# Performance work log

Measured on AMD Instinct MI355X. Metric: run time of the kernel, lower is better.

## Reference

```python
import jax, jax.numpy as jnp
import numpy as np

L, B, S, D, SD, E, V = 6, 16, 512, 512, 128, 1536, 32000
PDX = 1  # padding_idx: embedding row zeroed


def _pos_encode(seq_len, d_model):
    pos = np.arange(seq_len)[:, None].astype(np.float32)
    i = np.arange(d_model)[None, :].astype(np.float32)
    ang = pos / np.power(10000.0, 2.0 * np.floor(i / 2.0) / d_model)
    pe = np.where(np.arange(d_model)[None, :] % 2 == 0, np.sin(ang), np.cos(ang))
    return jnp.asarray(pe, dtype=jnp.float32)


def setup_inputs() -> dict:
    key = jax.random.key(0)
    ks = jax.random.split(key, 12)
    def n(k, shape, std=0.02):
        return jax.random.normal(k, shape, jnp.float32) * std
    embed = n(ks[0], (V, D)).at[PDX].set(0.0)
    return dict(
        src_tokens=jax.random.randint(ks[1], (B, S), 0, V),
        src_mask=jax.random.randint(ks[2], (B, S), 0, 2).astype(bool),
        embed=embed,
        ln_g=jnp.ones((L, D)), ln_b=jnp.zeros((L, D)),
        Wz=n(ks[3], (L, D, SD)), bz=jnp.zeros((L, SD)),
        gq=1.0 + n(ks[4], (L, S, SD)), bq=n(ks[5], (L, S, SD)),
        gk=1.0 + n(ks[6], (L, S, SD)), bk=n(ks[7], (L, S, SD)),
        Wu=n(ks[8], (L, D, E)), bu=jnp.zeros((L, E)),
        Wv=n(ks[9], (L, D, E)), bv=jnp.zeros((L, E)),
        Wo=n(ks[10], (L, E, D)), bo=jnp.zeros((L, D)),
        fin_g=jnp.ones((D,)), fin_b=jnp.zeros((D,)),
    )


def _ln(x, g, b, eps=1e-5):
    m = x.mean(-1, keepdims=True)
    v = ((x - m) ** 2).mean(-1, keepdims=True)
    return (x - m) * jax.lax.rsqrt(v + eps) * g + b


def reference(src_tokens, src_mask, embed, ln_g, ln_b, Wz, bz, gq, bq, gk, bk,
              Wu, bu, Wv, bv, Wo, bo, fin_g, fin_b):
    d_model = embed.shape[1]
    x = embed[src_tokens] * (d_model ** 0.5)
    x = x + _pos_encode(src_tokens.shape[1], d_model)[None]  # dropout: eval -> identity
    mask = src_mask[:, None, :]  # (B,1,S): zero attention to masked key positions

    def layer(x, p):
        lg, lb, wz, bz_, gq_, bq_, gk_, bk_, wu, bu_, wv, bv_, wo, bo_ = p
        xn = _ln(x, lg, lb)
        u = xn @ wu + bu_          # (B,S,E)
        v = xn @ wv + bv_          # (B,S,E)
        z = xn @ wz + bz_          # (B,S,SD)
        q = z * gq_ + bq_          # scale_offset (per-position affine)
        k = z * gk_ + bk_
        a = jnp.maximum(jnp.einsum('bsd,btd->bst', q, k), 0.0) ** 2  # relu(qk)^2
        a = jnp.where(mask, 0.0, a)
        o = u * jnp.einsum('bst,bte->bse', a, v)  # gated attention output
        return x + o @ wo + bo_, None

    params = (ln_g, ln_b, Wz, bz, gq, bq, gk, bk, Wu, bu, Wv, bv, Wo, bo)
    x, _ = jax.lax.scan(layer, x, params)
    return _ln(x, fin_g, fin_b)
```

## Files before the change

### kernel.cpp

```cpp
#include <hip/hip_runtime.h>
#include <hip/hip_bf16.h>
#include <stdint.h>

constexpr int L = 6, B = 16, S = 512, D = 512, SD = 128, E = 1536;

using bf16x8 = __attribute__((ext_vector_type(8))) short;
using f32x4  = __attribute__((ext_vector_type(4))) float;

typedef __attribute__((address_space(1))) void gvoid;
typedef __attribute__((address_space(3))) void lvoid;

__device__ __forceinline__ unsigned short f2bf(float f) {
    __hip_bfloat16 h = __float2bfloat16(f);
    return __builtin_bit_cast(unsigned short, h);
}
__device__ __forceinline__ float bf2f(unsigned short u) {
    unsigned int v = ((unsigned int)u) << 16;
    return __builtin_bit_cast(float, v);
}
__device__ __forceinline__ void gload16(const void* g, void* l) {
    __builtin_amdgcn_global_load_lds((gvoid*)g, (lvoid*)l, 16, 0, 0);
}

__device__ __forceinline__ void swz_bid(int& bx, int& by, int& bz) {
    int gx = gridDim.x, gy = gridDim.y, gz = gridDim.z;
    int n = gx * gy * gz;
    int id = blockIdx.x + gx * (blockIdx.y + gy * blockIdx.z);
    int id2 = (id & 7) * (n >> 3) + (id >> 3);
    by = id2 % gy;
    int t = id2 / gy;
    bx = t % gx;
    bz = t / gx;
}

__global__ void detect_mask_kernel(const unsigned char* __restrict__ m, int* flag) {
    if (threadIdx.x == 0) *flag = 0;
    __syncthreads();
    int any = 0;
    for (int i = threadIdx.x; i < B * S; i += blockDim.x)
        if ((i & 3) != 0 && m[i] != 0) any = 1;
    if (any) atomicOr(flag, 1);
}

__global__ void embed_kernel(const int* __restrict__ tok, const float* __restrict__ embed,
                             float* __restrict__ x) {
    int idx = blockIdx.x * blockDim.x + threadIdx.x;
    int d = idx & (D - 1);
    int bs = idx >> 9;
    int s = bs & (S - 1);
    float e = embed[(size_t)tok[bs] * D + d] * 22.62741699796952f;
    float expo = (float)(d >> 1) * (1.0f / 256.0f);
    float ang = (float)s * expf(expo * -9.210340371976184f);
    float pe = (d & 1) ? cosf(ang) : sinf(ang);
    x[idx] = e + pe;
}

__global__ __launch_bounds__(256) void tcast_kernel(const float* __restrict__ W,
                                                    unsigned short* __restrict__ Wt,
                                                    int K, int N, long ostride) {
    __shared__ float t[32][33];
    W  += (size_t)blockIdx.z * K * N;
    Wt += (size_t)blockIdx.z * ostride;
    int k0 = blockIdx.x * 32, n0 = blockIdx.y * 32;
    int tx = threadIdx.x, ty = threadIdx.y;
#pragma unroll
    for (int i = 0; i < 4; ++i)
        t[ty + i * 8][tx] = W[(size_t)(k0 + ty + i * 8) * N + n0 + tx];
    __syncthreads();
#pragma unroll
    for (int i = 0; i < 4; ++i)
        Wt[(size_t)(n0 + ty + i * 8) * K + k0 + tx] = f2bf(t[tx][ty + i * 8]);
}

template <bool BF>
__global__ __launch_bounds__(256) void ln_kernel(const float* __restrict__ x,
                                                 const float* __restrict__ g,
                                                 const float* __restrict__ b,
                                                 void* __restrict__ yp) {
    int row = blockIdx.x * 4 + (threadIdx.x >> 6);
    int lane = threadIdx.x & 63;
    const float* xr = x + (size_t)row * D;
    float4 v0 = *(const float4*)(xr + lane * 4);
    float4 v1 = *(const float4*)(xr + 256 + lane * 4);
    float sum = v0.x + v0.y + v0.z + v0.w + v1.x + v1.y + v1.z + v1.w;
#pragma unroll
    for (int o = 1; o < 64; o <<= 1) sum += __shfl_xor(sum, o);
    float m = sum * (1.0f / D);
    float d0 = v0.x - m, d1 = v0.y - m, d2 = v0.z - m, d3 = v0.w - m;
    float e0 = v1.x - m, e1 = v1.y - m, e2 = v1.z - m, e3 = v1.w - m;
    float sq = d0 * d0 + d1 * d1 + d2 * d2 + d3 * d3 + e0 * e0 + e1 * e1 + e2 * e2 + e3 * e3;
#pragma unroll
    for (int o = 1; o < 64; o <<= 1) sq += __shfl_xor(sq, o);
    float inv = rsqrtf(sq * (1.0f / D) + 1e-5f);
    int c0 = lane * 4, c1 = 256 + lane * 4;
    float4 g0 = *(const float4*)(g + c0), g1 = *(const float4*)(g + c1);
    float4 b0 = *(const float4*)(b + c0), b1 = *(const float4*)(b + c1);
    float o0 = d0 * inv * g0.x + b0.x, o1 = d1 * inv * g0.y + b0.y;
    float o2 = d2 * inv * g0.z + b0.z, o3 = d3 * inv * g0.w + b0.w;
    float o4 = e0 * inv * g1.x + b1.x, o5 = e1 * inv * g1.y + b1.y;
    float o6 = e2 * inv * g1.z + b1.z, o7 = e3 * inv * g1.w + b1.w;
    if constexpr (BF) {
        unsigned short* yr = (unsigned short*)yp + (size_t)row * D;
        ushort4 p0 = {f2bf(o0), f2bf(o1), f2bf(o2), f2bf(o3)};
        ushort4 p1 = {f2bf(o4), f2bf(o5), f2bf(o6), f2bf(o7)};
        *(ushort4*)(yr + c0) = p0;
        *(ushort4*)(yr + c1) = p1;
    } else {
        float* yr = (float*)yp + (size_t)row * D;
        float4 p0 = {o0, o1, o2, o3}, p1 = {o4, o5, o6, o7};
        *(float4*)(yr + c0) = p0;
        *(float4*)(yr + c1) = p1;
    }
}

template <int BM, int BN, bool SWAP>
__device__ __forceinline__ void gemm_core(const unsigned short* __restrict__ Ab,
                                          const unsigned short* __restrict__ Bb,
                                          int K, short* lsA, short* lsB,
                                          f32x4 (&acc)[BM / 32][BN / 32],
                                          int lane, int wv) {
    constexpr int NA = BM / 32, NB = BN / 32;
    constexpr int FM = BM / 32, FN = BN / 32;
    constexpr int WTM = BM / 2, WTN = BN / 2;
    const int wm = wv >> 1, wn = wv & 1;
    const unsigned short* ga[NA]; int lofsA[NA];
    const unsigned short* gb[NB]; int lofsB[NB];
#pragma unroll
    for (int i = 0; i < NA; ++i) {
        int s = wv * NA + i;
        int r = s * 8 + (lane >> 3);
        int cl = (lane & 7) ^ (r & 7);
        ga[i] = Ab + (size_t)r * K + cl * 8;
        lofsA[i] = s * 512;
    }
#pragma unroll
    for (int i = 0; i < NB; ++i) {
        int s = wv * NB + i;
        int r = s * 8 + (lane >> 3);
        int cl = (lane & 7) ^ (r & 7);
        gb[i] = Bb + (size_t)r * K + cl * 8;
        lofsB[i] = s * 512;
    }
    const int nkt = K >> 6;
    for (int kt = 0; kt < nkt; ++kt) {
        if (kt) __syncthreads();
#pragma unroll
        for (int i = 0; i < NA; ++i) gload16(ga[i] + kt * 64, (void*)&lsA[lofsA[i]]);
#pragma unroll
        for (int i = 0; i < NB; ++i) gload16(gb[i] + kt * 64, (void*)&lsB[lofsB[i]]);
        __syncthreads();
#pragma unroll
        for (int ks = 0; ks < 2; ++ks) {
            bf16x8 aF[FM], bF[FN];
#pragma unroll
            for (int f = 0; f < FM; ++f) {
                int ra = wm * WTM + f * 16 + (lane & 15);
                int ca = (ks * 4 + (lane >> 4)) ^ (ra & 7);
                aF[f] = *(const bf16x8*)&lsA[ra * 64 + ca * 8];
            }
#pragma unroll
            for (int f = 0; f < FN; ++f) {
                int rb = wn * WTN + f * 16 + (lane & 15);
                int cb = (ks * 4 + (lane >> 4)) ^ (rb & 7);
                bF[f] = *(const bf16x8*)&lsB[rb * 64 + cb * 8];
            }
#pragma unroll
            for (int fi = 0; fi < FM; ++fi)
#pragma unroll
                for (int fj = 0; fj < FN; ++fj) {
                    if constexpr (SWAP)
                        acc[fi][fj] = __builtin_amdgcn_mfma_f32_16x16x32_bf16(
                            bF[fj], aF[fi], acc[fi][fj], 0, 0, 0);
                    else
                        acc[fi][fj] = __builtin_amdgcn_mfma_f32_16x16x32_bf16(
                            aF[fi], bF[fj], acc[fi][fj], 0, 0, 0);
                }
        }
    }
}

__global__ __launch_bounds__(256) void uv_gemm(const unsigned short* __restrict__ xn,
                                               const unsigned short* __restrict__ Wuvt,
                                               const float* __restrict__ bu,
                                               const float* __restrict__ bvp,
                                               unsigned short* __restrict__ u,
                                               unsigned short* __restrict__ vt) {
    __shared__ short lsA[128 * 64];
    __shared__ short lsB[128 * 64];
    int bx, by, bz;
    swz_bid(bx, by, bz);
    const int tid = threadIdx.x;
    const int lane = tid & 63, wv = tid >> 6;
    const int wm = wv >> 1, wn = wv & 1;
    const int row0 = bx * 128, col0 = by * 128;
    const unsigned short* Ab = xn + (size_t)row0 * D;
    const unsigned short* Bb = Wuvt + ((size_t)bz * E + col0) * D;

    const int lr4 = (lane >> 4) * 4;
    const int lc = lane & 15;
    if (bz == 0) {
        f32x4 acc[4][4] = {};
        gemm_core<128, 128, true>(Ab, Bb, D, lsA, lsB, acc, lane, wv);
#pragma unroll
        for (int fi = 0; fi < 4; ++fi) {
            int r = row0 + wm * 64 + fi * 16 + lc;
#pragma unroll
            for (int fj = 0; fj < 4; ++fj) {
                int cb = col0 + wn * 64 + fj * 16 + lr4;
                f32x4 v = acc[fi][fj];
                f32x4 bv = *(const f32x4*)&bu[cb];
                ushort4 ov = {f2bf(v[0] + bv[0]), f2bf(v[1] + bv[1]),
                              f2bf(v[2] + bv[2]), f2bf(v[3] + bv[3])};
                *(ushort4*)&u[(size_t)r * E + cb] = ov;
            }
        }
    } else {
        f32x4 acc[4][4] = {};
        gemm_core<128, 128, false>(Ab, Bb, D, lsA, lsB, acc, lane, wv);
#pragma unroll
        for (int fi = 0; fi < 4; ++fi) {
            int rb = row0 + wm * 64 + fi * 16 + lr4;
#pragma unroll
            for (int fj = 0; fj < 4; ++fj) {
                int c = col0 + wn * 64 + fj * 16 + lc;
                f32x4 v = acc[fi][fj];
                float bv = bvp[c];
                int b = rb >> 9, t0 = rb & 511;
                ushort4 ov = {f2bf(v[0] + bv), f2bf(v[1] + bv),
                              f2bf(v[2] + bv), f2bf(v[3] + bv)};
                *(ushort4*)&vt[((size_t)b * E + c) * 512 + t0] = ov;
            }
        }
    }
}

__global__ __launch_bounds__(256) void zqk_gemm(const unsigned short* __restrict__ xn,
                                                const unsigned short* __restrict__ Bt,
                                                const float* __restrict__ bias,
                                                const float* __restrict__ gq,
                                                const float* __restrict__ bq,
                                                const float* __restrict__ gk,
                                                const float* __restrict__ bk,
                                                unsigned short* __restrict__ q,
                                                unsigned short* __restrict__ k) {
    __shared__ short lsA[128 * 64];
    __shared__ short lsB[128 * 64];
    int bx, by, bz;
    swz_bid(bx, by, bz);
    const int tid = threadIdx.x;
    const int lane = tid & 63, wv = tid >> 6;
    const int wm = wv >> 1, wn = wv & 1;
    const int row0 = bx * 128;
    const unsigned short* Ab = xn + (size_t)row0 * D;

    f32x4 acc[4][4] = {};
    gemm_core<128, 128, true>(Ab, Bt, D, lsA, lsB, acc, lane, wv);

    const int lr4 = (lane >> 4) * 4;
    const int lc = lane & 15;
#pragma unroll
    for (int fi = 0; fi < 4; ++fi) {
        int r = row0 + wm * 64 + fi * 16 + lc;
        int s = r & 511;
#pragma unroll
        for (int fj = 0; fj < 4; ++fj) {
            int cb = wn * 64 + fj * 16 + lr4;
            f32x4 v = acc[fi][fj];
            f32x4 bz4 = *(const f32x4*)&bias[cb];
            f32x4 gq4 = *(const f32x4*)&gq[(size_t)s * SD + cb];
            f32x4 bq4 = *(const f32x4*)&bq[(size_t)s * SD + cb];
            f32x4 gk4 = *(const f32x4*)&gk[(size_t)s * SD + cb];
            f32x4 bk4 = *(const f32x4*)&bk[(size_t)s * SD + cb];
            ushort4 qv, kv;
#pragma unroll
            for (int g = 0; g < 4; ++g) {
                float zz = v[g] + bz4[g];
                ((unsigned short*)&qv)[g] = f2bf(fmaf(zz, gq4[g], bq4[g]));
                ((unsigned short*)&kv)[g] = f2bf(fmaf(zz, gk4[g], bk4[g]));
            }
            *(ushort4*)&q[(size_t)r * SD + cb] = qv;
            *(ushort4*)&k[(size_t)r * SD + cb] = kv;
        }
    }
}

template <int EPI, int BM, int BN>
__global__ __launch_bounds__(256) void mgemm(const unsigned short* __restrict__ A,
                                             const unsigned short* __restrict__ Bt,
                                             const float* __restrict__ bias,
                                             const void* __restrict__ aux,
                                             const int* __restrict__ flagp,
                                             void* __restrict__ Cp,
                                             int N, int K,
                                             long sA, long sB, long sC, long sAux) {
    __shared__ short lsA[BM * 64];
    __shared__ short lsB[BN * 64];
    constexpr int FM = BM / 32, FN = BN / 32;
    int bx, by, bz;
    swz_bid(bx, by, bz);
    const int tid = threadIdx.x;
    const int lane = tid & 63, wv = tid >> 6;
    const int wm = wv >> 1, wn = wv & 1;
    const int row0 = bx * BM, col0 = by * BN;

    const unsigned short* Ab = A + (size_t)bz * sA + (size_t)row0 * K;
    const unsigned short* Bb = Bt + (size_t)bz * sB + (size_t)col0 * K;

    f32x4 acc[FM][FN] = {};
    gemm_core<BM, BN, true>(Ab, Bb, K, lsA, lsB, acc, lane, wv);

    const int lr4 = (lane >> 4) * 4;
    const int lc = lane & 15;
#pragma unroll
    for (int fi = 0; fi < FM; ++fi) {
        int r = row0 + wm * (BM / 2) + fi * 16 + lc;
#pragma unroll
        for (int fj = 0; fj < FN; ++fj) {
            int cb = col0 + wn * (BN / 2) + fj * 16 + lr4;
            f32x4 v = acc[fi][fj];
            if constexpr (EPI == 3) {
                unsigned short* C = (unsigned short*)Cp + (size_t)bz * sC;
                int flag = *flagp;
                ushort4 ov;
#pragma unroll
                for (int g = 0; g < 4; ++g) {
                    int c = cb + g;
                    int mv = flag ? (int)((const unsigned char*)aux)[bz * sAux + c]
                                  : ((const int*)aux)[bz * sAux + c];
                    float vv = fmaxf(v[g], 0.0f);
                    vv *= vv;
                    ((unsigned short*)&ov)[g] = mv ? (unsigned short)0 : f2bf(vv);
                }
                *(ushort4*)&C[(size_t)r * N + cb] = ov;
            } else if constexpr (EPI == 4) {
                const unsigned short* U = (const unsigned short*)aux + (size_t)bz * sAux;
                unsigned short* C = (unsigned short*)Cp + (size_t)bz * sC;
                size_t off = (size_t)r * N + cb;
                ushort4 uu = *(const ushort4*)&U[off];
                ushort4 ov = {f2bf(bf2f(uu.x) * v[0]), f2bf(bf2f(uu.y) * v[1]),
                              f2bf(bf2f(uu.z) * v[2]), f2bf(bf2f(uu.w) * v[3])};
                *(ushort4*)&C[off] = ov;
            } else {
                float* C = (float*)Cp;
                const float* X = (const float*)aux;
                size_t off = (size_t)r * N + cb;
                f32x4 bb = *(const f32x4*)&bias[cb];
                f32x4 xx = *(const f32x4*)&X[off];
                f32x4 ov = {v[0] + bb[0] + xx[0], v[1] + bb[1] + xx[1],
                            v[2] + bb[2] + xx[2], v[3] + bb[3] + xx[3]};
                *(f32x4*)&C[off] = ov;
            }
        }
    }
}

extern "C" void kernel_launch(void* const* d_in, const int* in_sizes, int n_in,
                              void* d_out, int out_size, void* d_ws, size_t ws_size,
                              hipStream_t stream) {
    const int* tok = (const int*)d_in[0];
    const unsigned char* mask = (const unsigned char*)d_in[1];
    const float* embed = (const float*)d_in[2];
    const float* ln_g = (const float*)d_in[3];
    const float* ln_b = (const float*)d_in[4];
    const float* Wz = (const float*)d_in[5];
    const float* bz = (const float*)d_in[6];
    const float* gq = (const float*)d_in[7];
    const float* bq = (const float*)d_in[8];
    const float* gk = (const float*)d_in[9];
    const float* bk = (const float*)d_in[10];
    const float* Wu = (const float*)d_in[11];
    const float* bu = (const float*)d_in[12];
    const float* Wv = (const float*)d_in[13];
    const float* bv = (const float*)d_in[14];
    const float* Wo = (const float*)d_in[15];
    const float* bo = (const float*)d_in[16];
    const float* fin_g = (const float*)d_in[17];
    const float* fin_b = (const float*)d_in[18];

    char* wsb = (char*)d_ws;
    size_t off = 0;
    auto alloc = [&](size_t nbytes) {
        void* p = wsb + off;
        off = (off + nbytes + 255) & ~(size_t)255;
        return p;
    };
    int* flag = (int*)alloc(256);
    float* x = (float*)alloc((size_t)B * S * D * 4);
    unsigned short* xn = (unsigned short*)alloc((size_t)B * S * D * 2);
    unsigned short* q = (unsigned short*)alloc((size_t)B * S * SD * 2);
    unsigned short* k = (unsigned short*)alloc((size_t)B * S * SD * 2);
    unsigned short* u = (unsigned short*)alloc((size_t)B * S * E * 2);
    unsigned short* vt = (unsigned short*)alloc((size_t)B * E * S * 2);
    unsigned short* o = (unsigned short*)alloc((size_t)B * S * E * 2);
    unsigned short* a = (unsigned short*)alloc((size_t)B * S * S * 2);
    unsigned short* Wuvzt = (unsigned short*)alloc((size_t)L * 3200 * D * 2);
    unsigned short* Wot = (unsigned short*)alloc((size_t)L * D * E * 2);

    constexpr long WUVZ = 3200L * D;

    detect_mask_kernel<<<1, 256, 0, stream>>>(mask, flag);
    embed_kernel<<<(B * S * D) / 256, 256, 0, stream>>>(tok, embed, x);
    tcast_kernel<<<dim3(D / 32, E / 32, L), dim3(32, 8), 0, stream>>>(Wu, Wuvzt, D, E, WUVZ);
    tcast_kernel<<<dim3(D / 32, E / 32, L), dim3(32, 8), 0, stream>>>(
        Wv, Wuvzt + 1536L * D, D, E, WUVZ);
    tcast_kernel<<<dim3(D / 32, SD / 32, L), dim3(32, 8), 0, stream>>>(
        Wz, Wuvzt + 3072L * D, D, SD, WUVZ);
    tcast_kernel<<<dim3(E / 32, D / 32, L), dim3(32, 8), 0, stream>>>(
        Wo, Wot, E, D, (long)D * E);

    for (int l = 0; l < L; ++l) {
        ln_kernel<true><<<B * S / 4, 256, 0, stream>>>(x, ln_g + l * D, ln_b + l * D, xn);
        uv_gemm<<<dim3(64, 12, 2), 256, 0, stream>>>(
            xn, Wuvzt + (size_t)l * WUVZ, bu + l * E, bv + l * E, u, vt);
        zqk_gemm<<<dim3(64, 1), 256, 0, stream>>>(
            xn, Wuvzt + (size_t)l * WUVZ + 3072L * D, bz + l * SD,
            gq + (size_t)l * S * SD, bq + (size_t)l * S * SD,
            gk + (size_t)l * S * SD, bk + (size_t)l * S * SD, q, k);
        mgemm<3, 64, 64><<<dim3(8, 8, B), 256, 0, stream>>>(
            q, k, nullptr, mask, flag, a, S, SD,
            (long)S * SD, (long)S * SD, (long)S * S, S);
        mgemm<4, 128, 128><<<dim3(4, 12, B), 256, 0, stream>>>(
            a, vt, nullptr, u, nullptr, o, E, S,
            (long)S * S, (long)E * S, (long)S * E, (long)S * E);
        mgemm<5, 128, 64><<<dim3(64, 8), 256, 0, stream>>>(
            o, Wot + (size_t)l * D * E, bo + l * D, x, nullptr, x, D, E, 0, 0, 0, 0);
    }
    ln_kernel<false><<<B * S / 4, 256, 0, stream>>>(x, fin_g, fin_b, (float*)d_out);
}
```

Before: 769.5 us.

## Merge weight casts, retile zqk GEMM, add dedicated single-pass score GEMM

```diff
diff --git a/kernel.cpp b/kernel.cpp
--- a/kernel.cpp
+++ b/kernel.cpp
@@ -55,21 +55,31 @@
     x[idx] = e + pe;
 }
 
-__global__ __launch_bounds__(256) void tcast_kernel(const float* __restrict__ W,
-                                                    unsigned short* __restrict__ Wt,
-                                                    int K, int N, long ostride) {
-    __shared__ float t[32][33];
-    W  += (size_t)blockIdx.z * K * N;
-    Wt += (size_t)blockIdx.z * ostride;
-    int k0 = blockIdx.x * 32, n0 = blockIdx.y * 32;
-    int tx = threadIdx.x, ty = threadIdx.y;
+__global__ __launch_bounds__(256) void tcast_all(const float* __restrict__ Wu,
+                                                 const float* __restrict__ Wv,
+                                                 const float* __restrict__ Wz,
+                                                 const float* __restrict__ Wo,
+                                                 unsigned short* __restrict__ Wuvzt,
+                                                 unsigned short* __restrict__ Wot) {
+    constexpr long WUVZ = 3200L * 512;
+    int l = blockIdx.z;
+    int t = blockIdx.x;
+    const float* src; unsigned short* dst; int K, N, r;
+    if (t < 768)       { r = t;        src = Wu + (size_t)l * 512 * 1536; dst = Wuvzt + (size_t)l * WUVZ;               K = 512;  N = 1536; }
+    else if (t < 1536) { r = t - 768;  src = Wv + (size_t)l * 512 * 1536; dst = Wuvzt + (size_t)l * WUVZ + 1536L * 512; K = 512;  N = 1536; }
+    else if (t < 1600) { r = t - 1536; src = Wz + (size_t)l * 512 * 128;  dst = Wuvzt + (size_t)l * WUVZ + 3072L * 512; K = 512;  N = 128;  }
+    else               { r = t - 1600; src = Wo + (size_t)l * 1536 * 512; dst = Wot + (size_t)l * 1536 * 512;           K = 1536; N = 512;  }
+    int kx = K / 32;
+    int k0 = (r % kx) * 32, n0 = (r / kx) * 32;
+    __shared__ float tb[32][33];
+    int tx = threadIdx.x & 31, ty = threadIdx.x >> 5;
 #pragma unroll
     for (int i = 0; i < 4; ++i)
-        t[ty + i * 8][tx] = W[(size_t)(k0 + ty + i * 8) * N + n0 + tx];
+        tb[ty + i * 8][tx] = src[(size_t)(k0 + ty + i * 8) * N + n0 + tx];
     __syncthreads();
 #pragma unroll
     for (int i = 0; i < 4; ++i)
-        Wt[(size_t)(n0 + ty + i * 8) * K + k0 + tx] = f2bf(t[tx][ty + i * 8]);
+        dst[(size_t)(n0 + ty + i * 8) * K + k0 + tx] = f2bf(tb[tx][ty + i * 8]);
 }
 
 template <bool BF>
@@ -113,16 +123,17 @@
     }
 }
 
-template <int BM, int BN, bool SWAP>
+template <int BM, int BN, int WM, int WN, bool SWAP>
 __device__ __forceinline__ void gemm_core(const unsigned short* __restrict__ Ab,
                                           const unsigned short* __restrict__ Bb,
                                           int K, short* lsA, short* lsB,
-                                          f32x4 (&acc)[BM / 32][BN / 32],
+                                          f32x4 (&acc)[BM / WM / 16][BN / WN / 16],
                                           int lane, int wv) {
-    constexpr int NA = BM / 32, NB = BN / 32;
-    constexpr int FM = BM / 32, FN = BN / 32;
-    constexpr int WTM = BM / 2, WTN = BN / 2;
-    const int wm = wv >> 1, wn = wv & 1;
+    constexpr int NW = WM * WN;
+    constexpr int NA = BM / 8 / NW, NB = BN / 8 / NW;
+    constexpr int WTM = BM / WM, WTN = BN / WN;
+    constexpr int FM = WTM / 16, FN = WTN / 16;
+    const int wm = wv / WN, wn = wv % WN;
     const unsigned short* ga[NA]; int lofsA[NA];
     const unsigned short* gb[NB]; int lofsB[NB];
 #pragma unroll
@@ -200,7 +211,7 @@
     const int lc = lane & 15;
     if (bz == 0) {
         f32x4 acc[4][4] = {};
-        gemm_core<128, 128, true>(Ab, Bb, D, lsA, lsB, acc, lane, wv);
+        gemm_core<128, 128, 2, 2, true>(Ab, Bb, D, lsA, lsB, acc, lane, wv);
 #pragma unroll
         for (int fi = 0; fi < 4; ++fi) {
             int r = row0 + wm * 64 + fi * 16 + lc;
@@ -216,7 +227,7 @@
         }
     } else {
         f32x4 acc[4][4] = {};
-        gemm_core<128, 128, false>(Ab, Bb, D, lsA, lsB, acc, lane, wv);
+        gemm_core<128, 128, 2, 2, false>(Ab, Bb, D, lsA, lsB, acc, lane, wv);
 #pragma unroll
         for (int fi = 0; fi < 4; ++fi) {
             int rb = row0 + wm * 64 + fi * 16 + lr4;
@@ -243,28 +254,29 @@
                                                 const float* __restrict__ bk,
                                                 unsigned short* __restrict__ q,
                                                 unsigned short* __restrict__ k) {
-    __shared__ short lsA[128 * 64];
-    __shared__ short lsB[128 * 64];
+    __shared__ short lsA[64 * 64];
+    __shared__ short lsB[64 * 64];
     int bx, by, bz;
     swz_bid(bx, by, bz);
     const int tid = threadIdx.x;
     const int lane = tid & 63, wv = tid >> 6;
     const int wm = wv >> 1, wn = wv & 1;
-    const int row0 = bx * 128;
+    const int row0 = bx * 64, col0 = by * 64;
     const unsigned short* Ab = xn + (size_t)row0 * D;
-
-    f32x4 acc[4][4] = {};
-    gemm_core<128, 128, true>(Ab, Bt, D, lsA, lsB, acc, lane, wv);
+    const unsigned short* Bb = Bt + (size_t)col0 * D;
+
+    f32x4 acc[2][2] = {};
+    gemm_core<64, 64, 2, 2, true>(Ab, Bb, D, lsA, lsB, acc, lane, wv);
 
     const int lr4 = (lane >> 4) * 4;
     const int lc = lane & 15;
 #pragma unroll
-    for (int fi = 0; fi < 4; ++fi) {
-        int r = row0 + wm * 64 + fi * 16 + lc;
+    for (int fi = 0; fi < 2; ++fi) {
+        int r = row0 + wm * 32 + fi * 16 + lc;
         int s = r & 511;
 #pragma unroll
-        for (int fj = 0; fj < 4; ++fj) {
-            int cb = wn * 64 + fj * 16 + lr4;
+        for (int fj = 0; fj < 2; ++fj) {
+            int cb = col0 + wn * 32 + fj * 16 + lr4;
             f32x4 v = acc[fi][fj];
             f32x4 bz4 = *(const f32x4*)&bias[cb];
             f32x4 gq4 = *(const f32x4*)&gq[(size_t)s * SD + cb];
@@ -284,7 +296,103 @@
     }
 }
 
-template <int EPI, int BM, int BN>
+__global__ __launch_bounds__(256) void score_gemm(const unsigned short* __restrict__ q,
+                                                  const unsigned short* __restrict__ km,
+                                                  const unsigned char* __restrict__ maskb,
+                                                  const int* __restrict__ flagp,
+                                                  unsigned short* __restrict__ a) {
+    __shared__ short lsA[2][128 * 64];
+    __shared__ short lsB[2][64 * 64];
+    int bx, by, bz;
+    swz_bid(bx, by, bz);
+    const int tid = threadIdx.x;
+    const int lane = tid & 63, wv = tid >> 6;
+    const int wm = wv >> 1, wn = wv & 1;
+    const int row0 = bx * 128, col0 = by * 64;
+    const unsigned short* Ab = q + (size_t)bz * S * SD + (size_t)row0 * SD;
+    const unsigned short* Bb = km + (size_t)bz * S * SD + (size_t)col0 * SD;
+
+    const unsigned short* ga[4]; int lofsA[4];
+    const unsigned short* gb[2]; int lofsB[2];
+#pragma unroll
+    for (int i = 0; i < 4; ++i) {
+        int s = wv * 4 + i;
+        int r = s * 8 + (lane >> 3);
+        int cl = (lane & 7) ^ (r & 7);
+        ga[i] = Ab + (size_t)r * SD + cl * 8;
+        lofsA[i] = s * 512;
+    }
+#pragma unroll
+    for (int i = 0; i < 2; ++i) {
+        int s = wv * 2 + i;
+        int r = s * 8 + (lane >> 3);
+        int cl = (lane & 7) ^ (r & 7);
+        gb[i] = Bb + (size_t)r * SD + cl * 8;
+        lofsB[i] = s * 512;
+    }
+#pragma unroll
+    for (int i = 0; i < 4; ++i) gload16(ga[i], (void*)&lsA[0][lofsA[i]]);
+#pragma unroll
+    for (int i = 0; i < 2; ++i) gload16(gb[i], (void*)&lsB[0][lofsB[i]]);
+#pragma unroll
+    for (int i = 0; i < 4; ++i) gload16(ga[i] + 64, (void*)&lsA[1][lofsA[i]]);
+#pragma unroll
+    for (int i = 0; i < 2; ++i) gload16(gb[i] + 64, (void*)&lsB[1][lofsB[i]]);
+    __syncthreads();
+
+    f32x4 acc[4][2] = {};
+#pragma unroll
+    for (int kt = 0; kt < 2; ++kt) {
+#pragma unroll
+        for (int ks = 0; ks < 2; ++ks) {
+            bf16x8 aF[4], bF[2];
+#pragma unroll
+            for (int f = 0; f < 4; ++f) {
+                int ra = wm * 64 + f * 16 + (lane & 15);
+                int ca = (ks * 4 + (lane >> 4)) ^ (ra & 7);
+                aF[f] = *(const bf16x8*)&lsA[kt][ra * 64 + ca * 8];
+            }
+#pragma unroll
+            for (int f = 0; f < 2; ++f) {
+                int rb = wn * 32 + f * 16 + (lane & 15);
+                int cb = (ks * 4 + (lane >> 4)) ^ (rb & 7);
+                bF[f] = *(const bf16x8*)&lsB[kt][rb * 64 + cb * 8];
+            }
+#pragma unroll
+            for (int fi = 0; fi < 4; ++fi)
+#pragma unroll
+                for (int fj = 0; fj < 2; ++fj)
+                    acc[fi][fj] = __builtin_amdgcn_mfma_f32_16x16x32_bf16(
+                        bF[fj], aF[fi], acc[fi][fj], 0, 0, 0);
+        }
+    }
+
+    const int lr4 = (lane >> 4) * 4;
+    const int lc = lane & 15;
+    unsigned short* C = a + (size_t)bz * S * S;
+    int flag = *flagp;
+#pragma unroll
+    for (int fi = 0; fi < 4; ++fi) {
+        int r = row0 + wm * 64 + fi * 16 + lc;
+#pragma unroll
+        for (int fj = 0; fj < 2; ++fj) {
+            int cb = col0 + wn * 32 + fj * 16 + lr4;
+            f32x4 v = acc[fi][fj];
+            ushort4 ov;
+#pragma unroll
+            for (int g = 0; g < 4; ++g) {
+                int c = cb + g;
+                int mv = flag ? (int)maskb[bz * S + c] : ((const int*)maskb)[bz * S + c];
+                float vv = fmaxf(v[g], 0.0f);
+                vv *= vv;
+                ((unsigned short*)&ov)[g] = mv ? (unsigned short)0 : f2bf(vv);
+            }
+            *(ushort4*)&C[(size_t)r * S + cb] = ov;
+        }
+    }
+}
+
+template <int EPI, int BM, int BN, int WM, int WN>
 __global__ __launch_bounds__(256) void mgemm(const unsigned short* __restrict__ A,
                                              const unsigned short* __restrict__ Bt,
                                              const float* __restrict__ bias,
@@ -295,44 +403,30 @@
                                              long sA, long sB, long sC, long sAux) {
     __shared__ short lsA[BM * 64];
     __shared__ short lsB[BN * 64];
-    constexpr int FM = BM / 32, FN = BN / 32;
+    constexpr int FM = BM / WM / 16, FN = BN / WN / 16;
     int bx, by, bz;
     swz_bid(bx, by, bz);
     const int tid = threadIdx.x;
     const int lane = tid & 63, wv = tid >> 6;
-    const int wm = wv >> 1, wn = wv & 1;
+    const int wm = wv / WN, wn = wv % WN;
     const int row0 = bx * BM, col0 = by * BN;
 
     const unsigned short* Ab = A + (size_t)bz * sA + (size_t)row0 * K;
     const unsigned short* Bb = Bt + (size_t)bz * sB + (size_t)col0 * K;
 
     f32x4 acc[FM][FN] = {};
-    gemm_core<BM, BN, true>(Ab, Bb, K, lsA, lsB, acc, lane, wv);
+    gemm_core<BM, BN, WM, WN, true>(Ab, Bb, K, lsA, lsB, acc, lane, wv);
 
     const int lr4 = (lane >> 4) * 4;
     const int lc = lane & 15;
 #pragma unroll
     for (int fi = 0; fi < FM; ++fi) {
-        int r = row0 + wm * (BM / 2) + fi * 16 + lc;
+        int r = row0 + wm * (BM / WM) + fi * 16 + lc;
 #pragma unroll
         for (int fj = 0; fj < FN; ++fj) {
-            int cb = col0 + wn * (BN / 2) + fj * 16 + lr4;
+            int cb = col0 + wn * (BN / WN) + fj * 16 + lr4;
             f32x4 v = acc[fi][fj];
-            if constexpr (EPI == 3) {
-                unsigned short* C = (unsigned short*)Cp + (size_t)bz * sC;
-                int flag = *flagp;
-                ushort4 ov;
-#pragma unroll
-                for (int g = 0; g < 4; ++g) {
-                    int c = cb + g;
-                    int mv = flag ? (int)((const unsigned char*)aux)[bz * sAux + c]
-                                  : ((const int*)aux)[bz * sAux + c];
-                    float vv = fmaxf(v[g], 0.0f);
-                    vv *= vv;
-                    ((unsigned short*)&ov)[g] = mv ? (unsigned short)0 : f2bf(vv);
-                }
-                *(ushort4*)&C[(size_t)r * N + cb] = ov;
-            } else if constexpr (EPI == 4) {
+            if constexpr (EPI == 4) {
                 const unsigned short* U = (const unsigned short*)aux + (size_t)bz * sAux;
                 unsigned short* C = (unsigned short*)Cp + (size_t)bz * sC;
                 size_t off = (size_t)r * N + cb;
@@ -400,29 +494,21 @@
 
     detect_mask_kernel<<<1, 256, 0, stream>>>(mask, flag);
     embed_kernel<<<(B * S * D) / 256, 256, 0, stream>>>(tok, embed, x);
-    tcast_kernel<<<dim3(D / 32, E / 32, L), dim3(32, 8), 0, stream>>>(Wu, Wuvzt, D, E, WUVZ);
-    tcast_kernel<<<dim3(D / 32, E / 32, L), dim3(32, 8), 0, stream>>>(
-        Wv, Wuvzt + 1536L * D, D, E, WUVZ);
-    tcast_kernel<<<dim3(D / 32, SD / 32, L), dim3(32, 8), 0, stream>>>(
-        Wz, Wuvzt + 3072L * D, D, SD, WUVZ);
-    tcast_kernel<<<dim3(E / 32, D / 32, L), dim3(32, 8), 0, stream>>>(
-        Wo, Wot, E, D, (long)D * E);
+    tcast_all<<<dim3(2368, 1, L), 256, 0, stream>>>(Wu, Wv, Wz, Wo, Wuvzt, Wot);
 
     for (int l = 0; l < L; ++l) {
         ln_kernel<true><<<B * S / 4, 256, 0, stream>>>(x, ln_g + l * D, ln_b + l * D, xn);
         uv_gemm<<<dim3(64, 12, 2), 256, 0, stream>>>(
             xn, Wuvzt + (size_t)l * WUVZ, bu + l * E, bv + l * E, u, vt);
-        zqk_gemm<<<dim3(64, 1), 256, 0, stream>>>(
+        zqk_gemm<<<dim3(128, 2), 256, 0, stream>>>(
             xn, Wuvzt + (size_t)l * WUVZ + 3072L * D, bz + l * SD,
             gq + (size_t)l * S * SD, bq + (size_t)l * S * SD,
             gk + (size_t)l * S * SD, bk + (size_t)l * S * SD, q, k);
-        mgemm<3, 64, 64><<<dim3(8, 8, B), 256, 0, stream>>>(
-            q, k, nullptr, mask, flag, a, S, SD,
-            (long)S * SD, (long)S * SD, (long)S * S, S);
-        mgemm<4, 128, 128><<<dim3(4, 12, B), 256, 0, stream>>>(
+        score_gemm<<<dim3(4, 8, B), 256, 0, stream>>>(q, k, mask, flag, a);
+        mgemm<4, 128, 128, 2, 2><<<dim3(4, 12, B), 256, 0, stream>>>(
             a, vt, nullptr, u, nullptr, o, E, S,
             (long)S * S, (long)E * S, (long)S * E, (long)S * E);
-        mgemm<5, 128, 64><<<dim3(64, 8), 256, 0, stream>>>(
+        mgemm<5, 128, 64, 2, 2><<<dim3(64, 8), 256, 0, stream>>>(
             o, Wot + (size_t)l * D * E, bo + l * D, x, nullptr, x, D, E, 0, 0, 0, 0);
     }
     ln_kernel<false><<<B * S / 4, 256, 0, stream>>>(x, fin_g, fin_b, (float*)d_out);
```

After: 723.7 us. 1.06x faster.
